# Kernel tuning notes

Hardware: AMD Instinct MI355X
Metric: run time of the kernel (lower is better)

## Reference

```python
import jax, jax.numpy as jnp
import numpy as np

N, E, L, F, HID, OUT = 20000, 200000, 5, 4, 128, 3


def _lin(x, w, b):
    # torch Linear convention: w is [out, in]
    return x @ w.T + b


def setup_inputs() -> dict:
    key = jax.random.key(0)
    ks = iter(jax.random.split(key, 40))
    nrm = lambda shape, s=0.05: jax.random.normal(next(ks), shape, dtype=jnp.float32) * s
    inp = {
        'x': jax.random.normal(next(ks), (N, L, F), dtype=jnp.float32),
        'edge_index': jax.random.randint(next(ks), (2, E), 0, N, dtype=jnp.int64),
        'edge_attr': jax.random.normal(next(ks), (E, F), dtype=jnp.float32),
        'batch': jnp.zeros((N,), dtype=jnp.int64),
        'node_type': jax.random.normal(next(ks), (N, 1), dtype=jnp.float32),
        # PastStateEncoder params
        'emb': nrm((L, F), 1.0),
        'conv_w': nrm((HID, 2 * F, 3)),  # Conv1d(8,128,3) OIW
        'conv_b': nrm((HID,)),
        # FusionLayer Linear(129,128)
        'fuse_w': nrm((HID, HID + 1)), 'fuse_b': nrm((HID,)),
        # gnn1 EdgeModel: Linear(2*128+4,128), Linear(128,128)
        'g1e_w1': nrm((HID, 2 * HID + F)), 'g1e_b1': nrm((HID,)),
        'g1e_w2': nrm((HID, HID)), 'g1e_b2': nrm((HID,)),
        # gnn1 NodeModel: Linear(256,128), Linear(128,128)
        'g1n_w1': nrm((HID, 2 * HID)), 'g1n_b1': nrm((HID,)),
        'g1n_w2': nrm((HID, HID)), 'g1n_b2': nrm((HID,)),
        # gnn2 EdgeModel: Linear(2*128+128,128), Linear(128,128)
        'g2e_w1': nrm((HID, 3 * HID)), 'g2e_b1': nrm((HID,)),
        'g2e_w2': nrm((HID, HID)), 'g2e_b2': nrm((HID,)),
        # gnn2 NodeModel
        'g2n_w1': nrm((HID, 2 * HID)), 'g2n_b1': nrm((HID,)),
        'g2n_w2': nrm((HID, HID)), 'g2n_b2': nrm((HID,)),
        # final_mlp: Linear(128,128), BN(128), Linear(128,3)
        'fm_w1': nrm((HID, HID)), 'fm_b1': nrm((HID,)),
        'bn_g': jnp.ones((HID,), dtype=jnp.float32), 'bn_b': jnp.zeros((HID,), dtype=jnp.float32),
        'fm_w2': nrm((OUT, HID)), 'fm_b2': nrm((OUT,)),
    }
    return inp


def _encoder(x, emb, conv_w, conv_b):
    # x: [N, L, F]; append learned positional embedding -> [N, L, 2F]
    n = x.shape[0]
    xe = jnp.concatenate([x, jnp.broadcast_to(emb[None], (n, L, F))], axis=-1)
    xc = xe.transpose(0, 2, 1)  # [N, 2F, L]
    y = jax.lax.conv_general_dilated(
        xc, conv_w, window_strides=(1,), padding=[(1, 1)],
        dimension_numbers=('NCW', 'OIW', 'NCW'))
    y = y + conv_b[None, :, None]
    return y.mean(axis=-1)  # [N, HID]


def _edge_mlp(src, dst, ea, w1, b1, w2, b2):
    h = jax.nn.relu(_lin(jnp.concatenate([src, dst, ea], axis=1), w1, b1))
    return _lin(h, w2, b2)


def _node_mlp(x_row, ea, w1, b1, w2, b2):
    h = jax.nn.relu(_lin(jnp.concatenate([x_row, ea], axis=1), w1, b1))
    return _lin(h, w2, b2)


def reference(x, edge_index, edge_attr, batch, node_type,
              emb, conv_w, conv_b, fuse_w, fuse_b,
              g1e_w1, g1e_b1, g1e_w2, g1e_b2, g1n_w1, g1n_b1, g1n_w2, g1n_b2,
              g2e_w1, g2e_b1, g2e_w2, g2e_b2, g2n_w1, g2n_b1, g2n_w2, g2n_b2,
              fm_w1, fm_b1, bn_g, bn_b, fm_w2, fm_b2):
    row, col = edge_index[0], edge_index[1]
    h = _encoder(x, emb, conv_w, conv_b)                     # [N,128]
    h = _lin(jnp.concatenate([h, node_type], axis=-1), fuse_w, fuse_b)  # [N,128]
    # gnn1 (MetaLayer: edge model then node model; node model here is per-edge)
    ea = _edge_mlp(h[row], h[col], edge_attr, g1e_w1, g1e_b1, g1e_w2, g1e_b2)  # [E,128]
    h = _node_mlp(h[row], ea, g1n_w1, g1n_b1, g1n_w2, g1n_b2)                  # [E,128]
    # gnn2 (h now lives on edges; indices < N <= E remain valid, matching torch)
    ea = _edge_mlp(h[row], h[col], ea, g2e_w1, g2e_b1, g2e_w2, g2e_b2)
    h = _node_mlp(h[row], ea, g2n_w1, g2n_b1, g2n_w2, g2n_b2)
    # final head on edge_attr: Linear -> BatchNorm1d (training stats) -> ReLU -> Linear
    z = _lin(ea, fm_w1, fm_b1)
    mu = z.mean(axis=0)
    var = z.var(axis=0)  # biased, matches torch BN normalization
    z = (z - mu) * jax.lax.rsqrt(var + 1e-5) * bn_g + bn_b
    z = jax.nn.relu(z)
    return _lin(z, fm_w2, fm_b2)  # [E,3]
```

## Files before the change

### kernel.cpp

```cpp
#include <hip/hip_runtime.h>

#define N_NODES 20000
#define N_EDGES 200000
#define HID 128
#define STR 136
#define NBLK 3125

typedef unsigned short u16;
using bf16x8 = __attribute__((ext_vector_type(8))) __bf16;
using f32x4  = __attribute__((ext_vector_type(4))) float;

__device__ __forceinline__ u16 f2bf(float f) {
  union { float f; unsigned u; } v; v.f = f;
  unsigned u = v.u;
  return (u16)((u + 0x7FFFu + ((u >> 16) & 1u)) >> 16);
}
__device__ __forceinline__ float bf2f(unsigned s) {
  union { unsigned u; float f; } v; v.u = s << 16;
  return v.f;
}
__device__ __forceinline__ bf16x8 ld8(const u16* p) { return *(const bf16x8*)p; }

__device__ __forceinline__ void zero_acc(f32x4 acc[4][2]) {
#pragma unroll
  for (int i = 0; i < 4; ++i) {
    acc[i][0] = (f32x4){0.f, 0.f, 0.f, 0.f};
    acc[i][1] = (f32x4){0.f, 0.f, 0.f, 0.f};
  }
}

template <int KSTEPS, typename AF>
__device__ __forceinline__ void wgemm(const u16* __restrict__ PW, AF afrag,
                                      f32x4 acc[4][2], int lane, int wave) {
  const u16* pb = PW + (wave * 2 * 64 + lane) * 8;
  bf16x8 b0[2], b1[2];
  b0[0] = ld8(pb);
  b1[0] = ld8(pb + 512);
#pragma unroll
  for (int ks = 0; ks < KSTEPS; ++ks) {
    const int cur = ks & 1, nxt = cur ^ 1;
    if (ks + 1 < KSTEPS) {
      b0[nxt] = ld8(pb + (ks + 1) * 4096);
      b1[nxt] = ld8(pb + (ks + 1) * 4096 + 512);
    }
#pragma unroll
    for (int mt = 0; mt < 4; ++mt) {
      bf16x8 a = afrag(ks, mt);
      acc[mt][0] = __builtin_amdgcn_mfma_f32_16x16x32_bf16(a, b0[cur], acc[mt][0], 0, 0, 0);
      acc[mt][1] = __builtin_amdgcn_mfma_f32_16x16x32_bf16(a, b1[cur], acc[mt][1], 0, 0, 0);
    }
  }
}

template <bool RELU>
__device__ __forceinline__ void epi_store(u16* buf, const f32x4 acc[4][2],
                                          const float* __restrict__ bias,
                                          int lane, int wave) {
  const int c = lane & 15, q = lane >> 4;
  const float bb0 = bias[wave * 32 + c], bb1 = bias[wave * 32 + 16 + c];
#pragma unroll
  for (int mt = 0; mt < 4; ++mt)
#pragma unroll
    for (int nt = 0; nt < 2; ++nt) {
      const float bb = nt ? bb1 : bb0;
      const int col = wave * 32 + nt * 16 + c;
#pragma unroll
      for (int r = 0; r < 4; ++r) {
        float v = acc[mt][nt][r] + bb;
        if (RELU) v = fmaxf(v, 0.f);
        buf[(mt * 16 + q * 4 + r) * STR + col] = f2bf(v);
      }
    }
}

__device__ __forceinline__ void flush_buf(const u16* buf, u16* __restrict__ gout,
                                          int e0, int tid) {
#pragma unroll
  for (int it = 0; it < 4; ++it) {
    int cid = tid + it * 256, e = cid >> 4, p = cid & 15;
    uint4 v = *(const uint4*)(buf + e * STR + p * 8);
    *(uint4*)(gout + (size_t)(e0 + e) * HID + p * 8) = v;
  }
}

__global__ void k_fold(const float* __restrict__ emb, const float* __restrict__ conv_w,
                       const float* __restrict__ conv_b, const float* __restrict__ fuse_w,
                       const float* __restrict__ fuse_b, float* __restrict__ Mt,
                       float* __restrict__ C0, float* __restrict__ Wnt) {
  __shared__ float Ash[128][21];
  int o = threadIdx.x;
  {
    float b0 = conv_b[o];
#pragma unroll
    for (int p = 0; p < 5; ++p) {
#pragma unroll
      for (int i = 0; i < 8; ++i) {
        float s = 0.f;
#pragma unroll
        for (int k = 0; k < 3; ++k) {
          int t = p + 1 - k;
          if (t >= 0 && t < 5) s += conv_w[(o * 8 + i) * 3 + k];
        }
        s *= 0.2f;
        if (i < 4) Ash[o][p * 4 + i] = s;
        else b0 += emb[p * 4 + (i - 4)] * s;
      }
    }
    Ash[o][20] = b0;
  }
  __syncthreads();
  float m[20];
#pragma unroll
  for (int qq = 0; qq < 20; ++qq) m[qq] = 0.f;
  float c0 = fuse_b[o];
  for (int j = 0; j < 128; ++j) {
    float w = fuse_w[o * 129 + j];
#pragma unroll
    for (int qq = 0; qq < 20; ++qq) m[qq] += w * Ash[j][qq];
    c0 += w * Ash[j][20];
  }
#pragma unroll
  for (int qq = 0; qq < 20; ++qq) Mt[qq * 128 + o] = m[qq];
  C0[o] = c0;
  Wnt[o] = fuse_w[o * 129 + 128];
}

__global__ void k_fold2(const float* __restrict__ w6, const float* __restrict__ b6,
                        const float* __restrict__ w7, const float* __restrict__ b7,
                        float* __restrict__ W67, float* __restrict__ b67) {
  int o = blockIdx.x;
  int k = threadIdx.x;
  float s = 0.f;
  for (int j = 0; j < 128; ++j) s += w7[o * 128 + j] * w6[j * 128 + k];
  W67[o * 128 + k] = s;
  if (k == 0) {
    float sb = 0.f;
    for (int j = 0; j < 128; ++j) sb += w7[o * 128 + j] * b6[j];
    b67[o] = sb + b7[o];
  }
}

struct PackArgs {
  const float* src[6];
  u16* dst[6];
  int Kin[6];
  int ksCum[7];
};

__global__ void k_pack(PackArgs pa) {
  int bk = blockIdx.x;
  int mi = 0;
  while (bk >= pa.ksCum[mi + 1]) ++mi;
  int ks = bk - pa.ksCum[mi];
  const float* W = pa.src[mi];
  u16* D = pa.dst[mi] + ks * 4096;
  int Kin = pa.Kin[mi];
#pragma unroll
  for (int t = 0; t < 16; ++t) {
    int el = t * 256 + (int)threadIdx.x;
    int j = el & 7, ln = (el >> 3) & 63, ntile = el >> 9;
    int k = ks * 32 + ((ln >> 4) << 3) + j;
    int n = ntile * 16 + (ln & 15);
    float v = (k < Kin) ? W[n * Kin + k] : 0.0f;
    D[el] = f2bf(v);
  }
}

__global__ __launch_bounds__(256) void k_encode(const float* __restrict__ x,
                                                const float* __restrict__ node_type,
                                                const float* __restrict__ Mt,
                                                const float* __restrict__ C0,
                                                const float* __restrict__ Wnt,
                                                u16* __restrict__ h2) {
  __shared__ float xs[2][20];
  int local = threadIdx.x >> 7, o = threadIdx.x & 127;
  int node = blockIdx.x * 2 + local;
  if (threadIdx.x < 40) {
    int nn = threadIdx.x / 20, qq = threadIdx.x % 20;
    xs[nn][qq] = x[(blockIdx.x * 2 + nn) * 20 + qq];
  }
  __syncthreads();
  float acc = C0[o] + Wnt[o] * node_type[node];
#pragma unroll
  for (int qq = 0; qq < 20; ++qq) acc += xs[local][qq] * Mt[qq * 128 + o];
  h2[node * HID + o] = f2bf(acc);
}

__global__ __launch_bounds__(256, 4) void k_gnn1(
    const int* __restrict__ eidx, const float* __restrict__ eattr,
    const u16* __restrict__ h2, const u16* __restrict__ pW1, const u16* __restrict__ pW2,
    const u16* __restrict__ pW3, const u16* __restrict__ pW4, const float* __restrict__ b1,
    const float* __restrict__ b2, const float* __restrict__ b3, const float* __restrict__ b4,
    u16* __restrict__ ea1, u16* __restrict__ h3) {
  __shared__ __align__(16) u16 B0[64 * STR], B1[64 * STR];
  const int tid = threadIdx.x, lane = tid & 63, wave = tid >> 6;
  const int e0 = blockIdx.x * 64;
  const int m = lane & 15, q = lane >> 4;
  const int aoff = m * STR + q * 8;
  const int* rowI = eidx;
  const int* colI = eidx + N_EDGES;
  const int idr = rowI[e0 + lane], idc = colI[e0 + lane];
  const u16* hrow = h2 + (size_t)idr * HID;
  const u16* hcol = h2 + (size_t)idc * HID;

#pragma unroll
  for (int it = 0; it < 8; ++it) {
    int g = wave * 8 + it;
    int p = g & 15;
    uint4 v = *(const uint4*)((g < 16 ? hrow : hcol) + p * 8);
    *(uint4*)((g < 16 ? B0 : B1) + lane * STR + p * 8) = v;
  }

  bf16x8 ef[4];
#pragma unroll
  for (int mt = 0; mt < 4; ++mt) {
    union { u16 s[8]; uint4 u; bf16x8 v; } t;
    t.u = make_uint4(0u, 0u, 0u, 0u);
    if (q == 0) {
      float4 a = *(const float4*)(eattr + (size_t)(e0 + mt * 16 + m) * 4);
      t.s[0] = f2bf(a.x); t.s[1] = f2bf(a.y); t.s[2] = f2bf(a.z); t.s[3] = f2bf(a.w);
    }
    ef[mt] = t.v;
  }
  __syncthreads();

  f32x4 acc[4][2];
  zero_acc(acc);
  wgemm<9>(pW1, [&](int ks, int mt) -> bf16x8 {
    if (ks < 4) return ld8(B0 + aoff + mt * 16 * STR + ks * 32);
    if (ks < 8) return ld8(B1 + aoff + mt * 16 * STR + (ks - 4) * 32);
    return ef[mt];
  }, acc, lane, wave);
  __syncthreads();
  epi_store<true>(B1, acc, b1, lane, wave);
  __syncthreads();

  zero_acc(acc);
  wgemm<4>(pW2, [&](int ks, int mt) -> bf16x8 {
    return ld8(B1 + aoff + mt * 16 * STR + ks * 32);
  }, acc, lane, wave);
  epi_store<false>(B0, acc, b2, lane, wave);
  __syncthreads();
  flush_buf(B0, ea1, e0, tid);

  if (e0 < N_NODES) {
#pragma unroll
    for (int it = 0; it < 4; ++it) {
      int p = wave * 4 + it;
      uint4 v = *(const uint4*)(hrow + p * 8);
      *(uint4*)(B1 + lane * STR + p * 8) = v;
    }
    __syncthreads();

    zero_acc(acc);
    wgemm<8>(pW3, [&](int ks, int mt) -> bf16x8 {
      if (ks < 4) return ld8(B1 + aoff + mt * 16 * STR + ks * 32);
      return ld8(B0 + aoff + mt * 16 * STR + (ks - 4) * 32);
    }, acc, lane, wave);
    __syncthreads();
    epi_store<true>(B1, acc, b3, lane, wave);
    __syncthreads();

    zero_acc(acc);
    wgemm<4>(pW4, [&](int ks, int mt) -> bf16x8 {
      return ld8(B1 + aoff + mt * 16 * STR + ks * 32);
    }, acc, lane, wave);
    epi_store<false>(B0, acc, b4, lane, wave);
    __syncthreads();
    flush_buf(B0, h3, e0, tid);
  }
}

__global__ __launch_bounds__(256, 4) void k_gnn2(
    const int* __restrict__ eidx, const u16* __restrict__ h3, u16* ea1z,
    const u16* __restrict__ pW5, const u16* __restrict__ pW67,
    const float* __restrict__ b5, const float* __restrict__ b67,
    float* __restrict__ partials) {
  __shared__ __align__(16) u16 B0[64 * STR], B1[64 * STR];
  const int tid = threadIdx.x, lane = tid & 63, wave = tid >> 6;
  const int e0 = blockIdx.x * 64;
  const int m = lane & 15, q = lane >> 4;
  const int aoff = m * STR + q * 8;
  const int* rowI = eidx;
  const int* colI = eidx + N_EDGES;
  const int idr = rowI[e0 + lane], idc = colI[e0 + lane];
  const u16* hrow = h3 + (size_t)idr * HID;
  const u16* hcol = h3 + (size_t)idc * HID;

#pragma unroll
  for (int it = 0; it < 8; ++it) {
    int g = wave * 8 + it;
    int p = g & 15;
    uint4 v = *(const uint4*)((g < 16 ? hrow : hcol) + p * 8);
    *(uint4*)((g < 16 ? B0 : B1) + lane * STR + p * 8) = v;
  }
  __syncthreads();

  f32x4 acc[4][2];
  zero_acc(acc);
  wgemm<8>(pW5, [&](int ks, int mt) -> bf16x8 {
    if (ks < 4) return ld8(B0 + aoff + mt * 16 * STR + ks * 32);
    return ld8(B1 + aoff + mt * 16 * STR + (ks - 4) * 32);
  }, acc, lane, wave);
  __syncthreads();

#pragma unroll
  for (int it = 0; it < 4; ++it) {
    int cid = tid + it * 256, e = cid >> 4, p = cid & 15;
    uint4 v = *(const uint4*)(ea1z + (size_t)(e0 + e) * HID + p * 8);
    *(uint4*)(B0 + e * STR + p * 8) = v;
  }
  __syncthreads();

  wgemm<4>(pW5 + 8 * 4096, [&](int ks, int mt) -> bf16x8 {
    return ld8(B0 + aoff + mt * 16 * STR + ks * 32);
  }, acc, lane, wave);
  epi_store<true>(B1, acc, b5, lane, wave);
  __syncthreads();

  zero_acc(acc);
  wgemm<4>(pW67, [&](int ks, int mt) -> bf16x8 {
    return ld8(B1 + aoff + mt * 16 * STR + ks * 32);
  }, acc, lane, wave);

  {
    const int c = lane & 15;
    const float bb0 = b67[wave * 32 + c], bb1 = b67[wave * 32 + 16 + c];
    float s0 = 0.f, q0 = 0.f, s1 = 0.f, q1 = 0.f;
#pragma unroll
    for (int mt = 0; mt < 4; ++mt)
#pragma unroll
      for (int r = 0; r < 4; ++r) {
        float v0 = acc[mt][0][r] + bb0;
        float v1 = acc[mt][1][r] + bb1;
        s0 += v0; q0 += v0 * v0;
        s1 += v1; q1 += v1 * v1;
        int row = mt * 16 + q * 4 + r;
        B0[row * STR + wave * 32 + c] = f2bf(v0);
        B0[row * STR + wave * 32 + 16 + c] = f2bf(v1);
      }
    s0 += __shfl_xor(s0, 16); s0 += __shfl_xor(s0, 32);
    q0 += __shfl_xor(q0, 16); q0 += __shfl_xor(q0, 32);
    s1 += __shfl_xor(s1, 16); s1 += __shfl_xor(s1, 32);
    q1 += __shfl_xor(q1, 16); q1 += __shfl_xor(q1, 32);
    if (lane < 16) {
      int base = (int)blockIdx.x * 256;
      partials[base + wave * 32 + lane] = s0;
      partials[base + wave * 32 + 16 + lane] = s1;
      partials[base + 128 + wave * 32 + lane] = q0;
      partials[base + 128 + wave * 32 + 16 + lane] = q1;
    }
  }
  __syncthreads();
  flush_buf(B0, ea1z, e0, tid);
}

__global__ void k_reduce(const float* __restrict__ partials, float* __restrict__ bnacc,
                         int nrows) {
  int t = threadIdx.x;
  float s = 0.f;
  for (int b = blockIdx.x; b < nrows; b += 64) s += partials[b * 256 + t];
  atomicAdd(&bnacc[t], s);
}

__global__ void k_bnfin(const float* __restrict__ bnacc, const float* __restrict__ bn_g,
                        const float* __restrict__ bn_b, float* __restrict__ ss) {
  int t = threadIdx.x;
  float inv = 1.0f / (float)N_EDGES;
  float mu = bnacc[t] * inv;
  float var = bnacc[128 + t] * inv - mu * mu;
  float sc = bn_g[t] * rsqrtf(var + 1e-5f);
  ss[t] = sc;
  ss[128 + t] = bn_b[t] - mu * sc;
}

__global__ __launch_bounds__(256) void k_head(const u16* __restrict__ z,
                                              const float* __restrict__ ss,
                                              const float* __restrict__ w2,
                                              const float* __restrict__ b2,
                                              float* __restrict__ out) {
  __shared__ float sh_s[128], sh_h[128], sh_w0[128], sh_w1[128], sh_w2[128];
  const int tid = threadIdx.x;
  if (tid < 128) {
    sh_s[tid] = ss[tid];
    sh_h[tid] = ss[128 + tid];
    sh_w0[tid] = w2[tid];
    sh_w1[tid] = w2[128 + tid];
    sh_w2[tid] = w2[256 + tid];
  }
  __syncthreads();
  const int e = blockIdx.x * 256 + tid;
  if (e >= N_EDGES) return;
  float a0 = b2[0], a1 = b2[1], a2 = b2[2];
  const u16* zr = z + (size_t)e * HID;
#pragma unroll
  for (int p = 0; p < 16; ++p) {
    uint4 v = *(const uint4*)(zr + p * 8);
    unsigned wv[4] = {v.x, v.y, v.z, v.w};
#pragma unroll
    for (int k = 0; k < 4; ++k) {
      int ch = p * 8 + k * 2;
      float lo = bf2f(wv[k] & 0xffffu), hi = bf2f(wv[k] >> 16);
      float r0 = fmaxf(fmaf(lo, sh_s[ch], sh_h[ch]), 0.f);
      float r1 = fmaxf(fmaf(hi, sh_s[ch + 1], sh_h[ch + 1]), 0.f);
      a0 += r0 * sh_w0[ch] + r1 * sh_w0[ch + 1];
      a1 += r0 * sh_w1[ch] + r1 * sh_w1[ch + 1];
      a2 += r0 * sh_w2[ch] + r1 * sh_w2[ch + 1];
    }
  }
  out[e * 3 + 0] = a0;
  out[e * 3 + 1] = a1;
  out[e * 3 + 2] = a2;
}

extern "C" void kernel_launch(void* const* d_in, const int* in_sizes, int n_in,
                              void* d_out, int out_size, void* d_ws, size_t ws_size,
                              hipStream_t stream) {
  const float* x         = (const float*)d_in[0];
  const int* eidx        = (const int*)d_in[1];
  const float* eattr     = (const float*)d_in[2];
  const float* node_type = (const float*)d_in[4];
  const float* emb       = (const float*)d_in[5];
  const float* conv_w    = (const float*)d_in[6];
  const float* conv_b    = (const float*)d_in[7];
  const float* fuse_w    = (const float*)d_in[8];
  const float* fuse_b    = (const float*)d_in[9];
  const float* g1e_w1    = (const float*)d_in[10];
  const float* g1e_b1    = (const float*)d_in[11];
  const float* g1e_w2    = (const float*)d_in[12];
  const float* g1e_b2    = (const float*)d_in[13];
  const float* g1n_w1    = (const float*)d_in[14];
  const float* g1n_b1    = (const float*)d_in[15];
  const float* g1n_w2    = (const float*)d_in[16];
  const float* g1n_b2    = (const float*)d_in[17];
  const float* g2e_w1    = (const float*)d_in[18];
  const float* g2e_b1    = (const float*)d_in[19];
  const float* g2e_w2    = (const float*)d_in[20];
  const float* g2e_b2    = (const float*)d_in[21];
  const float* fm_w1     = (const float*)d_in[26];
  const float* fm_b1     = (const float*)d_in[27];
  const float* bn_g      = (const float*)d_in[28];
  const float* bn_b      = (const float*)d_in[29];
  const float* fm_w2     = (const float*)d_in[30];
  const float* fm_b2     = (const float*)d_in[31];
  float* out = (float*)d_out;

  char* ws = (char*)d_ws;
  size_t off = 0;
  auto take = [&](size_t bytes) {
    void* p = ws + off;
    off = (off + bytes + 255) & ~(size_t)255;
    return p;
  };
  u16* h2   = (u16*)take((size_t)N_NODES * HID * 2);
  u16* h3   = (u16*)take((size_t)20032 * HID * 2);
  u16* ea1z = (u16*)take((size_t)N_EDGES * HID * 2);
  float* Mt    = (float*)take(20 * 128 * 4);
  float* C0    = (float*)take(128 * 4);
  float* Wnt   = (float*)take(128 * 4);
  float* bnacc = (float*)take(256 * 4);
  float* bnss  = (float*)take(256 * 4);
  float* W67f  = (float*)take(128 * 128 * 4);
  float* b67   = (float*)take(128 * 4);
  float* partials = (float*)take((size_t)NBLK * 256 * 4);
  u16* pW1  = (u16*)take(9 * 4096 * 2);
  u16* pW2  = (u16*)take(4 * 4096 * 2);
  u16* pW3  = (u16*)take(8 * 4096 * 2);
  u16* pW4  = (u16*)take(4 * 4096 * 2);
  u16* pW5  = (u16*)take(12 * 4096 * 2);
  u16* pW67 = (u16*)take(4 * 4096 * 2);

  hipMemsetAsync(bnacc, 0, 256 * 4, stream);
  k_fold<<<1, 128, 0, stream>>>(emb, conv_w, conv_b, fuse_w, fuse_b, Mt, C0, Wnt);
  k_fold2<<<128, 128, 0, stream>>>(g2e_w2, g2e_b2, fm_w1, fm_b1, W67f, b67);

  PackArgs pa;
  const float* srcs[6] = {g1e_w1, g1e_w2, g1n_w1, g1n_w2, g2e_w1, W67f};
  u16* dsts[6] = {pW1, pW2, pW3, pW4, pW5, pW67};
  int kins[6] = {260, 128, 256, 128, 384, 128};
  int kst[6] = {9, 4, 8, 4, 12, 4};
  int cum = 0;
  for (int i = 0; i < 6; ++i) {
    pa.src[i] = srcs[i]; pa.dst[i] = dsts[i]; pa.Kin[i] = kins[i];
    pa.ksCum[i] = cum; cum += kst[i];
  }
  pa.ksCum[6] = cum;
  k_pack<<<41, 256, 0, stream>>>(pa);

  k_encode<<<N_NODES / 2, 256, 0, stream>>>(x, node_type, Mt, C0, Wnt, h2);
  k_gnn1<<<NBLK, 256, 0, stream>>>(eidx, eattr, h2, pW1, pW2, pW3, pW4,
                                   g1e_b1, g1e_b2, g1n_b1, g1n_b2, ea1z, h3);
  k_gnn2<<<NBLK, 256, 0, stream>>>(eidx, h3, ea1z, pW5, pW67,
                                   g2e_b1, b67, partials);
  k_reduce<<<64, 256, 0, stream>>>(partials, bnacc, NBLK);
  k_bnfin<<<1, 128, 0, stream>>>(bnacc, bn_g, bn_b, bnss);
  k_head<<<(N_EDGES + 255) / 256, 256, 0, stream>>>(ea1z, bnss, fm_w2, fm_b2, out);
}
```

Before: 276.2 us.

## Cut kernel launches, coalesce row gathers, and batch nodes per block in encode

Folds the W67 product into the pack kernel and the bias fold into k_fold, dropping k_fold2. Replaces the per-block partials plus the k_reduce and k_bnfin kernels with direct atomicAdd into the BN accumulators, and moves the BN finalisation into k_head. Rewrites the edge gathers so that 16 lanes read one contiguous 256-byte row, and makes k_encode handle 16 nodes per block with Mt staged in shared memory and vector stores. The aim is fewer launches and better-coalesced memory access, at the cost of atomic contention and a nondeterministic summation order for the BN statistics.

```diff
diff --git a/kernel.cpp b/kernel.cpp
--- a/kernel.cpp
+++ b/kernel.cpp
@@ -83,10 +83,29 @@
   }
 }
 
+__device__ __forceinline__ void stage_gather(const int* __restrict__ rowI,
+                                             const int* __restrict__ colI,
+                                             const u16* __restrict__ htab,
+                                             u16* B0, u16* B1,
+                                             int e0, int lane, int wave) {
+  const int r = lane >> 4, p = lane & 15;
+#pragma unroll
+  for (int it = 0; it < 8; ++it) {
+    int j = wave * 32 + it * 4 + r;
+    int e = j & 63;
+    int id = (j < 64) ? rowI[e0 + e] : colI[e0 + e];
+    uint4 v = *(const uint4*)(htab + (size_t)id * HID + p * 8);
+    *(uint4*)(((j < 64) ? B0 : B1) + e * STR + p * 8) = v;
+  }
+}
+
 __global__ void k_fold(const float* __restrict__ emb, const float* __restrict__ conv_w,
                        const float* __restrict__ conv_b, const float* __restrict__ fuse_w,
-                       const float* __restrict__ fuse_b, float* __restrict__ Mt,
-                       float* __restrict__ C0, float* __restrict__ Wnt) {
+                       const float* __restrict__ fuse_b,
+                       const float* __restrict__ fm_w1, const float* __restrict__ g2e_b2,
+                       const float* __restrict__ fm_b1,
+                       float* __restrict__ Mt, float* __restrict__ C0,
+                       float* __restrict__ Wnt, float* __restrict__ b67) {
   __shared__ float Ash[128][21];
   int o = threadIdx.x;
   {
@@ -123,21 +142,9 @@
   for (int qq = 0; qq < 20; ++qq) Mt[qq * 128 + o] = m[qq];
   C0[o] = c0;
   Wnt[o] = fuse_w[o * 129 + 128];
-}
-
-__global__ void k_fold2(const float* __restrict__ w6, const float* __restrict__ b6,
-                        const float* __restrict__ w7, const float* __restrict__ b7,
-                        float* __restrict__ W67, float* __restrict__ b67) {
-  int o = blockIdx.x;
-  int k = threadIdx.x;
-  float s = 0.f;
-  for (int j = 0; j < 128; ++j) s += w7[o * 128 + j] * w6[j * 128 + k];
-  W67[o * 128 + k] = s;
-  if (k == 0) {
-    float sb = 0.f;
-    for (int j = 0; j < 128; ++j) sb += w7[o * 128 + j] * b6[j];
-    b67[o] = sb + b7[o];
-  }
+  float sb = 0.f;
+  for (int j = 0; j < 128; ++j) sb += fm_w1[o * 128 + j] * g2e_b2[j];
+  b67[o] = sb + fm_b1[o];
 }
 
 struct PackArgs {
@@ -145,6 +152,8 @@
   u16* dst[6];
   int Kin[6];
   int ksCum[7];
+  const float* w6;
+  const float* w7;
 };
 
 __global__ void k_pack(PackArgs pa) {
@@ -161,7 +170,14 @@
     int j = el & 7, ln = (el >> 3) & 63, ntile = el >> 9;
     int k = ks * 32 + ((ln >> 4) << 3) + j;
     int n = ntile * 16 + (ln & 15);
-    float v = (k < Kin) ? W[n * Kin + k] : 0.0f;
+    float v;
+    if (mi == 5) {
+      float s = 0.f;
+      for (int jj = 0; jj < 128; ++jj) s += pa.w7[n * 128 + jj] * pa.w6[jj * 128 + k];
+      v = s;
+    } else {
+      v = (k < Kin) ? W[n * Kin + k] : 0.0f;
+    }
     D[el] = f2bf(v);
   }
 }
@@ -172,18 +188,26 @@
                                                 const float* __restrict__ C0,
                                                 const float* __restrict__ Wnt,
                                                 u16* __restrict__ h2) {
-  __shared__ float xs[2][20];
-  int local = threadIdx.x >> 7, o = threadIdx.x & 127;
-  int node = blockIdx.x * 2 + local;
-  if (threadIdx.x < 40) {
-    int nn = threadIdx.x / 20, qq = threadIdx.x % 20;
-    xs[nn][qq] = x[(blockIdx.x * 2 + nn) * 20 + qq];
-  }
-  __syncthreads();
-  float acc = C0[o] + Wnt[o] * node_type[node];
-#pragma unroll
-  for (int qq = 0; qq < 20; ++qq) acc += xs[local][qq] * Mt[qq * 128 + o];
-  h2[node * HID + o] = f2bf(acc);
+  __shared__ float xs[16][20], nts[16], mts[20 * 128];
+  const int tid = threadIdx.x;
+  const int n0 = blockIdx.x * 16;
+  for (int i = tid; i < 320; i += 256) xs[i / 20][i % 20] = x[n0 * 20 + i];
+  if (tid < 16) nts[tid] = node_type[n0 + tid];
+  for (int i = tid; i < 2560; i += 256) mts[i] = Mt[i];
+  __syncthreads();
+  const int nl = tid >> 4;
+  const int c0 = (tid & 15) * 8;
+  float nt = nts[nl];
+  union { u16 s[8]; uint4 u; } o;
+#pragma unroll
+  for (int i = 0; i < 8; ++i) {
+    int ch = c0 + i;
+    float acc = C0[ch] + Wnt[ch] * nt;
+#pragma unroll
+    for (int qq = 0; qq < 20; ++qq) acc += xs[nl][qq] * mts[qq * 128 + ch];
+    o.s[i] = f2bf(acc);
+  }
+  *(uint4*)(h2 + (size_t)(n0 + nl) * HID + c0) = o.u;
 }
 
 __global__ __launch_bounds__(256, 4) void k_gnn1(
@@ -199,17 +223,8 @@
   const int aoff = m * STR + q * 8;
   const int* rowI = eidx;
   const int* colI = eidx + N_EDGES;
-  const int idr = rowI[e0 + lane], idc = colI[e0 + lane];
-  const u16* hrow = h2 + (size_t)idr * HID;
-  const u16* hcol = h2 + (size_t)idc * HID;
-
-#pragma unroll
-  for (int it = 0; it < 8; ++it) {
-    int g = wave * 8 + it;
-    int p = g & 15;
-    uint4 v = *(const uint4*)((g < 16 ? hrow : hcol) + p * 8);
-    *(uint4*)((g < 16 ? B0 : B1) + lane * STR + p * 8) = v;
-  }
+
+  stage_gather(rowI, colI, h2, B0, B1, e0, lane, wave);
 
   bf16x8 ef[4];
 #pragma unroll
@@ -246,9 +261,10 @@
   if (e0 < N_NODES) {
 #pragma unroll
     for (int it = 0; it < 4; ++it) {
-      int p = wave * 4 + it;
-      uint4 v = *(const uint4*)(hrow + p * 8);
-      *(uint4*)(B1 + lane * STR + p * 8) = v;
+      int e = wave * 16 + it * 4 + q;
+      int id = rowI[e0 + e];
+      uint4 v = *(const uint4*)(h2 + (size_t)id * HID + m * 8);
+      *(uint4*)(B1 + e * STR + m * 8) = v;
     }
     __syncthreads();
 
@@ -275,7 +291,7 @@
     const int* __restrict__ eidx, const u16* __restrict__ h3, u16* ea1z,
     const u16* __restrict__ pW5, const u16* __restrict__ pW67,
     const float* __restrict__ b5, const float* __restrict__ b67,
-    float* __restrict__ partials) {
+    float* __restrict__ bnacc) {
   __shared__ __align__(16) u16 B0[64 * STR], B1[64 * STR];
   const int tid = threadIdx.x, lane = tid & 63, wave = tid >> 6;
   const int e0 = blockIdx.x * 64;
@@ -283,17 +299,8 @@
   const int aoff = m * STR + q * 8;
   const int* rowI = eidx;
   const int* colI = eidx + N_EDGES;
-  const int idr = rowI[e0 + lane], idc = colI[e0 + lane];
-  const u16* hrow = h3 + (size_t)idr * HID;
-  const u16* hcol = h3 + (size_t)idc * HID;
-
-#pragma unroll
-  for (int it = 0; it < 8; ++it) {
-    int g = wave * 8 + it;
-    int p = g & 15;
-    uint4 v = *(const uint4*)((g < 16 ? hrow : hcol) + p * 8);
-    *(uint4*)((g < 16 ? B0 : B1) + lane * STR + p * 8) = v;
-  }
+
+  stage_gather(rowI, colI, h3, B0, B1, e0, lane, wave);
   __syncthreads();
 
   f32x4 acc[4][2];
@@ -344,46 +351,32 @@
     s1 += __shfl_xor(s1, 16); s1 += __shfl_xor(s1, 32);
     q1 += __shfl_xor(q1, 16); q1 += __shfl_xor(q1, 32);
     if (lane < 16) {
-      int base = (int)blockIdx.x * 256;
-      partials[base + wave * 32 + lane] = s0;
-      partials[base + wave * 32 + 16 + lane] = s1;
-      partials[base + 128 + wave * 32 + lane] = q0;
-      partials[base + 128 + wave * 32 + 16 + lane] = q1;
+      atomicAdd(&bnacc[wave * 32 + lane], s0);
+      atomicAdd(&bnacc[wave * 32 + 16 + lane], s1);
+      atomicAdd(&bnacc[128 + wave * 32 + lane], q0);
+      atomicAdd(&bnacc[128 + wave * 32 + 16 + lane], q1);
     }
   }
   __syncthreads();
   flush_buf(B0, ea1z, e0, tid);
 }
 
-__global__ void k_reduce(const float* __restrict__ partials, float* __restrict__ bnacc,
-                         int nrows) {
-  int t = threadIdx.x;
-  float s = 0.f;
-  for (int b = blockIdx.x; b < nrows; b += 64) s += partials[b * 256 + t];
-  atomicAdd(&bnacc[t], s);
-}
-
-__global__ void k_bnfin(const float* __restrict__ bnacc, const float* __restrict__ bn_g,
-                        const float* __restrict__ bn_b, float* __restrict__ ss) {
-  int t = threadIdx.x;
-  float inv = 1.0f / (float)N_EDGES;
-  float mu = bnacc[t] * inv;
-  float var = bnacc[128 + t] * inv - mu * mu;
-  float sc = bn_g[t] * rsqrtf(var + 1e-5f);
-  ss[t] = sc;
-  ss[128 + t] = bn_b[t] - mu * sc;
-}
-
 __global__ __launch_bounds__(256) void k_head(const u16* __restrict__ z,
-                                              const float* __restrict__ ss,
+                                              const float* __restrict__ bnacc,
+                                              const float* __restrict__ bn_g,
+                                              const float* __restrict__ bn_b,
                                               const float* __restrict__ w2,
                                               const float* __restrict__ b2,
                                               float* __restrict__ out) {
   __shared__ float sh_s[128], sh_h[128], sh_w0[128], sh_w1[128], sh_w2[128];
   const int tid = threadIdx.x;
   if (tid < 128) {
-    sh_s[tid] = ss[tid];
-    sh_h[tid] = ss[128 + tid];
+    const float inv = 1.0f / (float)N_EDGES;
+    float mu = bnacc[tid] * inv;
+    float var = bnacc[128 + tid] * inv - mu * mu;
+    float sc = bn_g[tid] * rsqrtf(var + 1e-5f);
+    sh_s[tid] = sc;
+    sh_h[tid] = bn_b[tid] - mu * sc;
     sh_w0[tid] = w2[tid];
     sh_w1[tid] = w2[128 + tid];
     sh_w2[tid] = w2[256 + tid];
@@ -459,10 +452,7 @@
   float* C0    = (float*)take(128 * 4);
   float* Wnt   = (float*)take(128 * 4);
   float* bnacc = (float*)take(256 * 4);
-  float* bnss  = (float*)take(256 * 4);
-  float* W67f  = (float*)take(128 * 128 * 4);
   float* b67   = (float*)take(128 * 4);
-  float* partials = (float*)take((size_t)NBLK * 256 * 4);
   u16* pW1  = (u16*)take(9 * 4096 * 2);
   u16* pW2  = (u16*)take(4 * 4096 * 2);
   u16* pW3  = (u16*)take(8 * 4096 * 2);
@@ -471,11 +461,11 @@
   u16* pW67 = (u16*)take(4 * 4096 * 2);
 
   hipMemsetAsync(bnacc, 0, 256 * 4, stream);
-  k_fold<<<1, 128, 0, stream>>>(emb, conv_w, conv_b, fuse_w, fuse_b, Mt, C0, Wnt);
-  k_fold2<<<128, 128, 0, stream>>>(g2e_w2, g2e_b2, fm_w1, fm_b1, W67f, b67);
+  k_fold<<<1, 128, 0, stream>>>(emb, conv_w, conv_b, fuse_w, fuse_b,
+                                fm_w1, g2e_b2, fm_b1, Mt, C0, Wnt, b67);
 
   PackArgs pa;
-  const float* srcs[6] = {g1e_w1, g1e_w2, g1n_w1, g1n_w2, g2e_w1, W67f};
+  const float* srcs[6] = {g1e_w1, g1e_w2, g1n_w1, g1n_w2, g2e_w1, nullptr};
   u16* dsts[6] = {pW1, pW2, pW3, pW4, pW5, pW67};
   int kins[6] = {260, 128, 256, 128, 384, 128};
   int kst[6] = {9, 4, 8, 4, 12, 4};
@@ -485,14 +475,15 @@
     pa.ksCum[i] = cum; cum += kst[i];
   }
   pa.ksCum[6] = cum;
+  pa.w6 = g2e_w2;
+  pa.w7 = fm_w1;
   k_pack<<<41, 256, 0, stream>>>(pa);
 
-  k_encode<<<N_NODES / 2, 256, 0, stream>>>(x, node_type, Mt, C0, Wnt, h2);
+  k_encode<<<N_NODES / 16, 256, 0, stream>>>(x, node_type, Mt, C0, Wnt, h2);
   k_gnn1<<<NBLK, 256, 0, stream>>>(eidx, eattr, h2, pW1, pW2, pW3, pW4,
                                    g1e_b1, g1e_b2, g1n_b1, g1n_b2, ea1z, h3);
   k_gnn2<<<NBLK, 256, 0, stream>>>(eidx, h3, ea1z, pW5, pW67,
-                                   g2e_b1, b67, partials);
-  k_reduce<<<64, 256, 0, stream>>>(partials, bnacc, NBLK);
-  k_bnfin<<<1, 128, 0, stream>>>(bnacc, bn_g, bn_b, bnss);
-  k_head<<<(N_EDGES + 255) / 256, 256, 0, stream>>>(ea1z, bnss, fm_w2, fm_b2, out);
-}
+                                   g2e_b1, b67, bnacc);
+  k_head<<<(N_EDGES + 255) / 256, 256, 0, stream>>>(ea1z, bnacc, bn_g, bn_b,
+                                                    fm_w2, fm_b2, out);
+}
```

Result: slower. 350.2 us (+26.8%).
